# Performance work log

Measured on AMD Instinct MI355X. Metric: run time of the kernel, lower is better.

## Reference

```python
import jax, jax.numpy as jnp
import numpy as np

DIM = 768
HEADS = 12
HIDDEN = 4 * DIM
B, N = 8, 1024
EPS = 1e-5


def setup_inputs() -> dict:
    key = jax.random.key(0)
    ks = jax.random.split(key, 8)
    s = 0.02
    return {
        "x": jax.random.normal(ks[0], (B, N, DIM), dtype=jnp.float32),
        "ln1_g": jnp.ones((DIM,), jnp.float32),
        "ln1_b": jnp.zeros((DIM,), jnp.float32),
        "qkv_w": jax.random.normal(ks[1], (3 * DIM, DIM), jnp.float32) * s,
        "proj_w": jax.random.normal(ks[2], (DIM, DIM), jnp.float32) * s,
        "proj_b": jnp.zeros((DIM,), jnp.float32),
        "ln2_g": jnp.ones((DIM,), jnp.float32),
        "ln2_b": jnp.zeros((DIM,), jnp.float32),
        "fc1_w": jax.random.normal(ks[3], (HIDDEN, DIM), jnp.float32) * s,
        "fc1_b": jnp.zeros((HIDDEN,), jnp.float32),
        "fc2_w": jax.random.normal(ks[4], (DIM, HIDDEN), jnp.float32) * s,
        "fc2_b": jnp.zeros((DIM,), jnp.float32),
    }


def _layernorm(x, g, b):
    mu = jnp.mean(x, axis=-1, keepdims=True)
    var = jnp.mean(jnp.square(x - mu), axis=-1, keepdims=True)
    return (x - mu) * jax.lax.rsqrt(var + EPS) * g + b


def reference(x, ln1_g, ln1_b, qkv_w, proj_w, proj_b, ln2_g, ln2_b, fc1_w, fc1_b, fc2_w, fc2_b):
    Bn, Nn, C = x.shape
    H = HEADS
    D = C // H
    scale = D ** -0.5

    # --- attention branch ---
    h = _layernorm(x, ln1_g, ln1_b)
    qkv = h @ qkv_w.T                      # [B,N,3C] (qkv_bias=False)
    qkv = qkv.reshape(Bn, Nn, 3, H, D)
    q = qkv[:, :, 0].transpose(0, 2, 1, 3)  # [B,H,N,D]
    k = qkv[:, :, 1].transpose(0, 2, 1, 3)
    v = qkv[:, :, 2].transpose(0, 2, 1, 3)
    attn = jnp.einsum('bhnd,bhmd->bhnm', q, k) * scale  # [B,H,N,N]
    attn = jax.nn.softmax(attn, axis=-1)
    ctx = jnp.einsum('bhnm,bhmd->bhnd', attn, v)         # [B,H,N,D]
    ctx = ctx.transpose(0, 2, 1, 3).reshape(Bn, Nn, C)
    x = x + ctx @ proj_w.T + proj_b

    # --- MLP branch ---
    h = _layernorm(x, ln2_g, ln2_b)
    h = jax.nn.gelu(h @ fc1_w.T + fc1_b, approximate=False)
    return x + h @ fc2_w.T + fc2_b
```

## Files before the change

### kernel.cpp

```cpp
#include <hip/hip_runtime.h>
#include <cstdint>

typedef __attribute__((ext_vector_type(8))) short short8;
typedef __attribute__((ext_vector_type(4))) float f32x4;
typedef unsigned short u16t;

__device__ __forceinline__ u16t f2bf(float f) {
  uint32_t u = __float_as_uint(f);
  u += 0x7fffu + ((u >> 16) & 1u);
  return (u16t)(u >> 16);
}

__device__ __forceinline__ uint32_t cvtpk(float lo, float hi) {
  uint32_t r;
  asm("v_cvt_pk_bf16_f32 %0, %1, %2" : "=v"(r) : "v"(lo), "v"(hi));
  return r;
}

__device__ __forceinline__ void gload_lds16(const void* g, void* l) {
  __builtin_amdgcn_global_load_lds(
      (const __attribute__((address_space(1))) void*)g,
      (__attribute__((address_space(3))) void*)l, 16, 0, 0);
}

__global__ __launch_bounds__(256) void cvt_bf16_kernel(const float* __restrict__ in,
                                                       u16t* __restrict__ out, int n8) {
  int i = blockIdx.x * 256 + threadIdx.x;
  if (i >= n8) return;
  const float4* p = (const float4*)in + (size_t)i * 2;
  float4 a = p[0], b = p[1];
  union { short8 v; u16t e[8]; } r;
  r.e[0] = f2bf(a.x); r.e[1] = f2bf(a.y); r.e[2] = f2bf(a.z); r.e[3] = f2bf(a.w);
  r.e[4] = f2bf(b.x); r.e[5] = f2bf(b.y); r.e[6] = f2bf(b.z); r.e[7] = f2bf(b.w);
  *((short8*)out + i) = r.v;
}

__global__ __launch_bounds__(256) void ln_kernel(const float* __restrict__ x,
                                                 const float* __restrict__ g,
                                                 const float* __restrict__ b,
                                                 u16t* __restrict__ out) {
  int row = blockIdx.x, tid = threadIdx.x;
  int wave = tid >> 6, lane = tid & 63;
  const float* xr = x + (size_t)row * 768;
  float v0 = xr[tid], v1 = xr[tid + 256], v2 = xr[tid + 512];
  float s = v0 + v1 + v2;
  float q = v0 * v0 + v1 * v1 + v2 * v2;
#pragma unroll
  for (int m = 32; m >= 1; m >>= 1) {
    s += __shfl_xor(s, m, 64);
    q += __shfl_xor(q, m, 64);
  }
  __shared__ float red[8];
  if (lane == 0) { red[wave] = s; red[4 + wave] = q; }
  __syncthreads();
  s = red[0] + red[1] + red[2] + red[3];
  q = red[4] + red[5] + red[6] + red[7];
  float mu = s * (1.0f / 768.0f);
  float var = q * (1.0f / 768.0f) - mu * mu;
  float rs = rsqrtf(var + 1e-5f);
  u16t* orow = out + (size_t)row * 768;
  orow[tid]       = f2bf((v0 - mu) * rs * g[tid]       + b[tid]);
  orow[tid + 256] = f2bf((v1 - mu) * rs * g[tid + 256] + b[tid + 256]);
  orow[tid + 512] = f2bf((v2 - mu) * rs * g[tid + 512] + b[tid + 512]);
}

template <int EPI, int BM>
__global__ __launch_bounds__(256, 2) void gemm_bt(const u16t* __restrict__ A,
                                                  const u16t* __restrict__ W,
                                                  void* __restrict__ Cout,
                                                  const float* __restrict__ bias,
                                                  const float* __restrict__ res,
                                                  int M, int N, int K) {
  __shared__ __align__(16) u16t As[BM * 64];
  __shared__ __align__(16) u16t Bs[128 * 64];
  constexpr int MF = BM / 32;
  int tid = threadIdx.x;
  int wave = tid >> 6, lane = tid & 63;
  int wr = wave >> 1, wc = wave & 1;
  int bm = blockIdx.y * BM;
  int bn = blockIdx.x * 128;
  f32x4 acc[MF][4] = {};

  int lr = lane >> 3;
  int lc = lane & 7;
  int srcslot = lc ^ lr;
  const u16t* Abase = A + (size_t)(bm + lr) * K + srcslot * 8;
  const u16t* Wbase = W + (size_t)(bn + lr) * K + srcslot * 8;

  for (int kt = 0; kt < K; kt += 64) {
    __syncthreads();
#pragma unroll
    for (int i = 0; i < BM / 32; i++) {
      int chunk = wave * (BM / 32) + i;
      gload_lds16(Abase + (size_t)(chunk * 8) * K + kt, (void*)(As + chunk * 512));
    }
#pragma unroll
    for (int i = 0; i < 4; i++) {
      int chunk = wave * 4 + i;
      gload_lds16(Wbase + (size_t)(chunk * 8) * K + kt, (void*)(Bs + chunk * 512));
    }
    __syncthreads();

    short8 af[MF][2], bfr[4][2];
#pragma unroll
    for (int m = 0; m < MF; m++) {
      int row = wr * (BM / 2) + m * 16 + (lane & 15);
#pragma unroll
      for (int s = 0; s < 2; s++) {
        int slot = s * 4 + (lane >> 4);
        af[m][s] = *(const short8*)(As + row * 64 + ((slot ^ (row & 7)) * 8));
      }
    }
#pragma unroll
    for (int n = 0; n < 4; n++) {
      int row = wc * 64 + n * 16 + (lane & 15);
#pragma unroll
      for (int s = 0; s < 2; s++) {
        int slot = s * 4 + (lane >> 4);
        bfr[n][s] = *(const short8*)(Bs + row * 64 + ((slot ^ (row & 7)) * 8));
      }
    }
    __builtin_amdgcn_s_setprio(1);
#pragma unroll
    for (int m = 0; m < MF; m++)
#pragma unroll
      for (int n = 0; n < 4; n++) {
        acc[m][n] = __builtin_amdgcn_mfma_f32_16x16x32_bf16(af[m][0], bfr[n][0], acc[m][n], 0, 0, 0);
        acc[m][n] = __builtin_amdgcn_mfma_f32_16x16x32_bf16(af[m][1], bfr[n][1], acc[m][n], 0, 0, 0);
      }
    __builtin_amdgcn_s_setprio(0);
  }

#pragma unroll
  for (int m = 0; m < MF; m++) {
#pragma unroll
    for (int n = 0; n < 4; n++) {
      int r0 = bm + wr * (BM / 2) + m * 16 + (lane >> 4) * 4;
      int c = bn + wc * 64 + n * 16 + (lane & 15);
#pragma unroll
      for (int i = 0; i < 4; i++) {
        int r = r0 + i;
        float v = acc[m][n][i];
        if constexpr (EPI == 0) {
          ((u16t*)Cout)[(size_t)r * N + c] = f2bf(v);
        } else if constexpr (EPI == 1) {
          ((float*)Cout)[(size_t)r * N + c] = v + bias[c] + res[(size_t)r * N + c];
        } else {
          v += bias[c];
          float gl = 0.5f * v * (1.0f + erff(v * 0.70710678118f));
          ((u16t*)Cout)[(size_t)r * N + c] = f2bf(gl);
        }
      }
    }
  }
}

__global__ __launch_bounds__(256) void vtrans_kernel(const u16t* __restrict__ qkv,
                                                     u16t* __restrict__ vt) {
  __shared__ u16t T[64][66];
  int h = blockIdx.x % 12, bb = blockIdx.x / 12, kt = blockIdx.y * 64;
  int t = threadIdx.x;
  int r = t >> 2, dc = t & 3;
  const u16t* src = qkv + (size_t)(bb * 1024 + kt + r) * 2304 + 1536 + h * 64 + dc * 16;
  union { uint4 u[2]; u16t e[16]; uint32_t w[8]; } buf;
  buf.u[0] = *(const uint4*)src;
  buf.u[1] = *(const uint4*)(src + 8);
#pragma unroll
  for (int j = 0; j < 8; j++)
    *(uint32_t*)&T[r][dc * 16 + 2 * j] = buf.w[j];
  __syncthreads();
  int d = t >> 2, kc = t & 3;
  union { uint4 u[2]; u16t e[16]; } o;
#pragma unroll
  for (int j = 0; j < 16; j++) o.e[j] = T[kc * 16 + j][d];
  u16t* dst = vt + ((size_t)blockIdx.x * 64 + d) * 1024 + kt + kc * 16;
  *(uint4*)dst = o.u[0];
  *(uint4*)(dst + 8) = o.u[1];
}

__global__ __launch_bounds__(256, 3) void attn_kernel(const u16t* __restrict__ qkv,
                                                      const u16t* __restrict__ vt,
                                                      u16t* __restrict__ ctx) {
  __shared__ __align__(16) u16t Plds[4][32 * 72];
  int tid = threadIdx.x;
  int wave = tid >> 6, lane = tid & 63;
  int q = lane & 15, g = lane >> 4;

  int bid = blockIdx.x;
  int xcd = bid & 7, j = bid >> 3;
  int head = xcd + 8 * (j >> 3);
  int qt = (j & 7) * 128 + wave * 32;
  int b = head / 12, h = head % 12;

  const u16t* base = qkv + (size_t)b * 1024 * 2304 + h * 64;
  const u16t* kbase = base + 768;
  const u16t* vtb = vt + (size_t)head * 64 * 1024;

  short8 qf[2][2];
#pragma unroll
  for (int hf = 0; hf < 2; hf++)
#pragma unroll
    for (int hh = 0; hh < 2; hh++)
      qf[hf][hh] = *(const short8*)(base + (size_t)(qt + hf * 16 + q) * 2304 + hh * 32 + g * 8);

  float mA = -1e30f, mB = -1e30f, lA = 0.f, lB = 0.f;
  f32x4 oA[4] = {}, oB[4] = {};
  u16t* Pw = Plds[wave];

  for (int kt = 0; kt < 1024; kt += 64) {
    short8 kf[4][2], vf[4][2];
#pragma unroll
    for (int n = 0; n < 4; n++)
#pragma unroll
      for (int hh = 0; hh < 2; hh++)
        kf[n][hh] = *(const short8*)(kbase + (size_t)(kt + n * 16 + q) * 2304 + hh * 32 + g * 8);
#pragma unroll
    for (int n = 0; n < 4; n++)
#pragma unroll
      for (int hh = 0; hh < 2; hh++)
        vf[n][hh] = *(const short8*)(vtb + (size_t)(n * 16 + q) * 1024 + kt + hh * 32 + g * 8);

    f32x4 sA[4] = {}, sB[4] = {};
    __builtin_amdgcn_s_setprio(1);
#pragma unroll
    for (int n = 0; n < 4; n++) {
      sA[n] = __builtin_amdgcn_mfma_f32_16x16x32_bf16(kf[n][0], qf[0][0], sA[n], 0, 0, 0);
      sA[n] = __builtin_amdgcn_mfma_f32_16x16x32_bf16(kf[n][1], qf[0][1], sA[n], 0, 0, 0);
      sB[n] = __builtin_amdgcn_mfma_f32_16x16x32_bf16(kf[n][0], qf[1][0], sB[n], 0, 0, 0);
      sB[n] = __builtin_amdgcn_mfma_f32_16x16x32_bf16(kf[n][1], qf[1][1], sB[n], 0, 0, 0);
    }
    __builtin_amdgcn_s_setprio(0);

    float alphaA, alphaB;
    {
      float tm = sA[0][0];
#pragma unroll
      for (int n = 0; n < 4; n++)
#pragma unroll
        for (int i = 0; i < 4; i++) tm = fmaxf(tm, sA[n][i]);
      tm = fmaxf(tm, __shfl_xor(tm, 16, 64));
      tm = fmaxf(tm, __shfl_xor(tm, 32, 64));
      float mnew = fmaxf(mA, tm);
      alphaA = __expf((mA - mnew) * 0.125f);
      mA = mnew;
      float rs = 0.f;
#pragma unroll
      for (int n = 0; n < 4; n++)
#pragma unroll
        for (int i = 0; i < 4; i++) {
          float p = __expf((sA[n][i] - mnew) * 0.125f);
          sA[n][i] = p;
          rs += p;
        }
      rs += __shfl_xor(rs, 16, 64);
      rs += __shfl_xor(rs, 32, 64);
      lA = lA * alphaA + rs;
#pragma unroll
      for (int n = 0; n < 4; n++) {
        uint32_t w0 = cvtpk(sA[n][0], sA[n][1]);
        uint32_t w1 = cvtpk(sA[n][2], sA[n][3]);
        *(uint2*)(Pw + q * 72 + n * 16 + g * 4) = make_uint2(w0, w1);
      }
    }
    {
      float tm = sB[0][0];
#pragma unroll
      for (int n = 0; n < 4; n++)
#pragma unroll
        for (int i = 0; i < 4; i++) tm = fmaxf(tm, sB[n][i]);
      tm = fmaxf(tm, __shfl_xor(tm, 16, 64));
      tm = fmaxf(tm, __shfl_xor(tm, 32, 64));
      float mnew = fmaxf(mB, tm);
      alphaB = __expf((mB - mnew) * 0.125f);
      mB = mnew;
      float rs = 0.f;
#pragma unroll
      for (int n = 0; n < 4; n++)
#pragma unroll
        for (int i = 0; i < 4; i++) {
          float p = __expf((sB[n][i] - mnew) * 0.125f);
          sB[n][i] = p;
          rs += p;
        }
      rs += __shfl_xor(rs, 16, 64);
      rs += __shfl_xor(rs, 32, 64);
      lB = lB * alphaB + rs;
#pragma unroll
      for (int n = 0; n < 4; n++) {
        uint32_t w0 = cvtpk(sB[n][0], sB[n][1]);
        uint32_t w1 = cvtpk(sB[n][2], sB[n][3]);
        *(uint2*)(Pw + (16 + q) * 72 + n * 16 + g * 4) = make_uint2(w0, w1);
      }
    }

#pragma unroll
    for (int n = 0; n < 4; n++)
#pragma unroll
      for (int i = 0; i < 4; i++) {
        oA[n][i] *= alphaA;
        oB[n][i] *= alphaB;
      }

    short8 pA[2], pB[2];
#pragma unroll
    for (int hh = 0; hh < 2; hh++) {
      pA[hh] = *(const short8*)(Pw + q * 72 + hh * 32 + g * 8);
      pB[hh] = *(const short8*)(Pw + (16 + q) * 72 + hh * 32 + g * 8);
    }
    __builtin_amdgcn_s_setprio(1);
#pragma unroll
    for (int n = 0; n < 4; n++)
#pragma unroll
      for (int hh = 0; hh < 2; hh++) {
        oA[n] = __builtin_amdgcn_mfma_f32_16x16x32_bf16(vf[n][hh], pA[hh], oA[n], 0, 0, 0);
        oB[n] = __builtin_amdgcn_mfma_f32_16x16x32_bf16(vf[n][hh], pB[hh], oB[n], 0, 0, 0);
      }
    __builtin_amdgcn_s_setprio(0);
  }

  float invA = 1.f / lA, invB = 1.f / lB;
  u16t* crowA = ctx + (size_t)(b * 1024 + qt + q) * 768 + h * 64;
  u16t* crowB = ctx + (size_t)(b * 1024 + qt + 16 + q) * 768 + h * 64;
#pragma unroll
  for (int n = 0; n < 4; n++) {
    uint32_t a0 = (uint32_t)f2bf(oA[n][0] * invA) | ((uint32_t)f2bf(oA[n][1] * invA) << 16);
    uint32_t a1 = (uint32_t)f2bf(oA[n][2] * invA) | ((uint32_t)f2bf(oA[n][3] * invA) << 16);
    *(uint32_t*)(crowA + n * 16 + g * 4) = a0;
    *(uint32_t*)(crowA + n * 16 + g * 4 + 2) = a1;
    uint32_t b0 = (uint32_t)f2bf(oB[n][0] * invB) | ((uint32_t)f2bf(oB[n][1] * invB) << 16);
    uint32_t b1 = (uint32_t)f2bf(oB[n][2] * invB) | ((uint32_t)f2bf(oB[n][3] * invB) << 16);
    *(uint32_t*)(crowB + n * 16 + g * 4) = b0;
    *(uint32_t*)(crowB + n * 16 + g * 4 + 2) = b1;
  }
}

extern "C" void kernel_launch(void* const* d_in, const int* in_sizes, int n_in,
                              void* d_out, int out_size, void* d_ws, size_t ws_size,
                              hipStream_t stream) {
  const float* x      = (const float*)d_in[0];
  const float* ln1_g  = (const float*)d_in[1];
  const float* ln1_b  = (const float*)d_in[2];
  const float* qkv_w  = (const float*)d_in[3];
  const float* proj_w = (const float*)d_in[4];
  const float* proj_b = (const float*)d_in[5];
  const float* ln2_g  = (const float*)d_in[6];
  const float* ln2_b  = (const float*)d_in[7];
  const float* fc1_w  = (const float*)d_in[8];
  const float* fc1_b  = (const float*)d_in[9];
  const float* fc2_w  = (const float*)d_in[10];
  const float* fc2_b  = (const float*)d_in[11];

  char* ws = (char*)d_ws;
  u16t* h1   = (u16t*)(ws + 0);
  u16t* qkvb = (u16t*)(ws + 12582912);
  u16t* ctx  = (u16t*)(ws + 50331648);
  float* x2  = (float*)(ws + 62914560);
  u16t* hid  = (u16t*)(ws + 88080384);
  u16t* wq   = (u16t*)(ws + 138412032);
  u16t* wp   = (u16t*)(ws + 141950976);
  u16t* w1   = (u16t*)(ws + 143130624);
  u16t* w2   = (u16t*)(ws + 147849216);
  u16t* vtb  = h1;
  float* out = (float*)d_out;

  cvt_bf16_kernel<<<864, 256, 0, stream>>>(qkv_w, wq, 221184);
  cvt_bf16_kernel<<<288, 256, 0, stream>>>(proj_w, wp, 73728);
  cvt_bf16_kernel<<<1152, 256, 0, stream>>>(fc1_w, w1, 294912);
  cvt_bf16_kernel<<<1152, 256, 0, stream>>>(fc2_w, w2, 294912);

  ln_kernel<<<8192, 256, 0, stream>>>(x, ln1_g, ln1_b, h1);
  gemm_bt<0, 128><<<dim3(18, 64), 256, 0, stream>>>(h1, wq, qkvb, nullptr, nullptr, 8192, 2304, 768);
  vtrans_kernel<<<dim3(96, 16), 256, 0, stream>>>(qkvb, vtb);
  attn_kernel<<<768, 256, 0, stream>>>(qkvb, vtb, ctx);
  gemm_bt<1, 64><<<dim3(6, 128), 256, 0, stream>>>(ctx, wp, x2, proj_b, x, 8192, 768, 768);
  ln_kernel<<<8192, 256, 0, stream>>>(x2, ln2_g, ln2_b, h1);
  gemm_bt<2, 128><<<dim3(24, 64), 256, 0, stream>>>(h1, w1, hid, fc1_b, nullptr, 8192, 3072, 768);
  gemm_bt<1, 64><<<dim3(6, 128), 256, 0, stream>>>(hid, w2, out, fc2_b, x2, 8192, 768, 3072);
}
```

Baseline: 306.5 us.

## Halve attention rows per wave and raise occupancy bounds for attention and GEMMs

Each attention wave now handles 16 query rows instead of 32, doubling the grid and cutting register and LDS use, which permits 4 blocks per CU. The V fragment loads are moved after the QK MFMAs, and the max and sum reductions become trees. GEMM launch bounds are made template parameters and raised to 3 or 4 blocks per CU. The cost is that K and V are reloaded twice as often per query, and the tighter register caps risk spills in the GEMMs.

After: 410.8 us. +34.0%, slower.

```diff
diff --git a/kernel.cpp b/kernel.cpp
--- a/kernel.cpp
+++ b/kernel.cpp
@@ -64,13 +64,13 @@
   orow[tid + 512] = f2bf((v2 - mu) * rs * g[tid + 512] + b[tid + 512]);
 }
 
-template <int EPI, int BM>
-__global__ __launch_bounds__(256, 2) void gemm_bt(const u16t* __restrict__ A,
-                                                  const u16t* __restrict__ W,
-                                                  void* __restrict__ Cout,
-                                                  const float* __restrict__ bias,
-                                                  const float* __restrict__ res,
-                                                  int M, int N, int K) {
+template <int EPI, int BM, int MINB>
+__global__ __launch_bounds__(256, MINB) void gemm_bt(const u16t* __restrict__ A,
+                                                     const u16t* __restrict__ W,
+                                                     void* __restrict__ Cout,
+                                                     const float* __restrict__ bias,
+                                                     const float* __restrict__ res,
+                                                     int M, int N, int K) {
   __shared__ __align__(16) u16t As[BM * 64];
   __shared__ __align__(16) u16t Bs[128 * 64];
   constexpr int MF = BM / 32;
@@ -178,159 +178,114 @@
   *(uint4*)(dst + 8) = o.u[1];
 }
 
-__global__ __launch_bounds__(256, 3) void attn_kernel(const u16t* __restrict__ qkv,
+__global__ __launch_bounds__(256, 4) void attn_kernel(const u16t* __restrict__ qkv,
                                                       const u16t* __restrict__ vt,
                                                       u16t* __restrict__ ctx) {
-  __shared__ __align__(16) u16t Plds[4][32 * 72];
+  __shared__ __align__(16) u16t Plds[4][16 * 72];
   int tid = threadIdx.x;
   int wave = tid >> 6, lane = tid & 63;
   int q = lane & 15, g = lane >> 4;
 
   int bid = blockIdx.x;
   int xcd = bid & 7, j = bid >> 3;
-  int head = xcd + 8 * (j >> 3);
-  int qt = (j & 7) * 128 + wave * 32;
+  int head = xcd + 8 * (j >> 4);
+  int qt = (j & 15) * 64 + wave * 16;
   int b = head / 12, h = head % 12;
 
   const u16t* base = qkv + (size_t)b * 1024 * 2304 + h * 64;
   const u16t* kbase = base + 768;
   const u16t* vtb = vt + (size_t)head * 64 * 1024;
 
-  short8 qf[2][2];
-#pragma unroll
-  for (int hf = 0; hf < 2; hf++)
-#pragma unroll
-    for (int hh = 0; hh < 2; hh++)
-      qf[hf][hh] = *(const short8*)(base + (size_t)(qt + hf * 16 + q) * 2304 + hh * 32 + g * 8);
-
-  float mA = -1e30f, mB = -1e30f, lA = 0.f, lB = 0.f;
-  f32x4 oA[4] = {}, oB[4] = {};
+  short8 qf[2];
+#pragma unroll
+  for (int hh = 0; hh < 2; hh++)
+    qf[hh] = *(const short8*)(base + (size_t)(qt + q) * 2304 + hh * 32 + g * 8);
+
+  float m_ = -1e30f, l_ = 0.f;
+  f32x4 o[4] = {};
   u16t* Pw = Plds[wave];
 
   for (int kt = 0; kt < 1024; kt += 64) {
-    short8 kf[4][2], vf[4][2];
+    short8 kf[4][2];
 #pragma unroll
     for (int n = 0; n < 4; n++)
 #pragma unroll
       for (int hh = 0; hh < 2; hh++)
         kf[n][hh] = *(const short8*)(kbase + (size_t)(kt + n * 16 + q) * 2304 + hh * 32 + g * 8);
+
+    f32x4 s[4] = {};
+    __builtin_amdgcn_s_setprio(1);
+#pragma unroll
+    for (int n = 0; n < 4; n++) {
+      s[n] = __builtin_amdgcn_mfma_f32_16x16x32_bf16(kf[n][0], qf[0], s[n], 0, 0, 0);
+      s[n] = __builtin_amdgcn_mfma_f32_16x16x32_bf16(kf[n][1], qf[1], s[n], 0, 0, 0);
+    }
+    __builtin_amdgcn_s_setprio(0);
+
+    short8 vf[4][2];
 #pragma unroll
     for (int n = 0; n < 4; n++)
 #pragma unroll
       for (int hh = 0; hh < 2; hh++)
         vf[n][hh] = *(const short8*)(vtb + (size_t)(n * 16 + q) * 1024 + kt + hh * 32 + g * 8);
 
-    f32x4 sA[4] = {}, sB[4] = {};
+    float tn0 = fmaxf(fmaxf(s[0][0], s[0][1]), fmaxf(s[0][2], s[0][3]));
+    float tn1 = fmaxf(fmaxf(s[1][0], s[1][1]), fmaxf(s[1][2], s[1][3]));
+    float tn2 = fmaxf(fmaxf(s[2][0], s[2][1]), fmaxf(s[2][2], s[2][3]));
+    float tn3 = fmaxf(fmaxf(s[3][0], s[3][1]), fmaxf(s[3][2], s[3][3]));
+    float tm = fmaxf(fmaxf(tn0, tn1), fmaxf(tn2, tn3));
+    tm = fmaxf(tm, __shfl_xor(tm, 16, 64));
+    tm = fmaxf(tm, __shfl_xor(tm, 32, 64));
+    float mnew = fmaxf(m_, tm);
+    float alpha = __expf((m_ - mnew) * 0.125f);
+    m_ = mnew;
+#pragma unroll
+    for (int n = 0; n < 4; n++)
+#pragma unroll
+      for (int i = 0; i < 4; i++)
+        s[n][i] = __expf((s[n][i] - mnew) * 0.125f);
+    float r0 = (s[0][0] + s[0][1]) + (s[0][2] + s[0][3]);
+    float r1 = (s[1][0] + s[1][1]) + (s[1][2] + s[1][3]);
+    float r2 = (s[2][0] + s[2][1]) + (s[2][2] + s[2][3]);
+    float r3 = (s[3][0] + s[3][1]) + (s[3][2] + s[3][3]);
+    float rs = (r0 + r1) + (r2 + r3);
+    rs += __shfl_xor(rs, 16, 64);
+    rs += __shfl_xor(rs, 32, 64);
+    l_ = l_ * alpha + rs;
+
+#pragma unroll
+    for (int n = 0; n < 4; n++) {
+      uint32_t w0 = cvtpk(s[n][0], s[n][1]);
+      uint32_t w1 = cvtpk(s[n][2], s[n][3]);
+      *(uint2*)(Pw + q * 72 + n * 16 + g * 4) = make_uint2(w0, w1);
+    }
+
+#pragma unroll
+    for (int n = 0; n < 4; n++)
+#pragma unroll
+      for (int i = 0; i < 4; i++) o[n][i] *= alpha;
+
+    short8 pA[2];
+#pragma unroll
+    for (int hh = 0; hh < 2; hh++)
+      pA[hh] = *(const short8*)(Pw + q * 72 + hh * 32 + g * 8);
     __builtin_amdgcn_s_setprio(1);
 #pragma unroll
     for (int n = 0; n < 4; n++) {
-      sA[n] = __builtin_amdgcn_mfma_f32_16x16x32_bf16(kf[n][0], qf[0][0], sA[n], 0, 0, 0);
-      sA[n] = __builtin_amdgcn_mfma_f32_16x16x32_bf16(kf[n][1], qf[0][1], sA[n], 0, 0, 0);
-      sB[n] = __builtin_amdgcn_mfma_f32_16x16x32_bf16(kf[n][0], qf[1][0], sB[n], 0, 0, 0);
-      sB[n] = __builtin_amdgcn_mfma_f32_16x16x32_bf16(kf[n][1], qf[1][1], sB[n], 0, 0, 0);
+      o[n] = __builtin_amdgcn_mfma_f32_16x16x32_bf16(vf[n][0], pA[0], o[n], 0, 0, 0);
+      o[n] = __builtin_amdgcn_mfma_f32_16x16x32_bf16(vf[n][1], pA[1], o[n], 0, 0, 0);
     }
     __builtin_amdgcn_s_setprio(0);
-
-    float alphaA, alphaB;
-    {
-      float tm = sA[0][0];
-#pragma unroll
-      for (int n = 0; n < 4; n++)
-#pragma unroll
-        for (int i = 0; i < 4; i++) tm = fmaxf(tm, sA[n][i]);
-      tm = fmaxf(tm, __shfl_xor(tm, 16, 64));
-      tm = fmaxf(tm, __shfl_xor(tm, 32, 64));
-      float mnew = fmaxf(mA, tm);
-      alphaA = __expf((mA - mnew) * 0.125f);
-      mA = mnew;
-      float rs = 0.f;
-#pragma unroll
-      for (int n = 0; n < 4; n++)
-#pragma unroll
-        for (int i = 0; i < 4; i++) {
-          float p = __expf((sA[n][i] - mnew) * 0.125f);
-          sA[n][i] = p;
-          rs += p;
-        }
-      rs += __shfl_xor(rs, 16, 64);
-      rs += __shfl_xor(rs, 32, 64);
-      lA = lA * alphaA + rs;
-#pragma unroll
-      for (int n = 0; n < 4; n++) {
-        uint32_t w0 = cvtpk(sA[n][0], sA[n][1]);
-        uint32_t w1 = cvtpk(sA[n][2], sA[n][3]);
-        *(uint2*)(Pw + q * 72 + n * 16 + g * 4) = make_uint2(w0, w1);
-      }
-    }
-    {
-      float tm = sB[0][0];
-#pragma unroll
-      for (int n = 0; n < 4; n++)
-#pragma unroll
-        for (int i = 0; i < 4; i++) tm = fmaxf(tm, sB[n][i]);
-      tm = fmaxf(tm, __shfl_xor(tm, 16, 64));
-      tm = fmaxf(tm, __shfl_xor(tm, 32, 64));
-      float mnew = fmaxf(mB, tm);
-      alphaB = __expf((mB - mnew) * 0.125f);
-      mB = mnew;
-      float rs = 0.f;
-#pragma unroll
-      for (int n = 0; n < 4; n++)
-#pragma unroll
-        for (int i = 0; i < 4; i++) {
-          float p = __expf((sB[n][i] - mnew) * 0.125f);
-          sB[n][i] = p;
-          rs += p;
-        }
-      rs += __shfl_xor(rs, 16, 64);
-      rs += __shfl_xor(rs, 32, 64);
-      lB = lB * alphaB + rs;
-#pragma unroll
-      for (int n = 0; n < 4; n++) {
-        uint32_t w0 = cvtpk(sB[n][0], sB[n][1]);
-        uint32_t w1 = cvtpk(sB[n][2], sB[n][3]);
-        *(uint2*)(Pw + (16 + q) * 72 + n * 16 + g * 4) = make_uint2(w0, w1);
-      }
-    }
-
-#pragma unroll
-    for (int n = 0; n < 4; n++)
-#pragma unroll
-      for (int i = 0; i < 4; i++) {
-        oA[n][i] *= alphaA;
-        oB[n][i] *= alphaB;
-      }
-
-    short8 pA[2], pB[2];
-#pragma unroll
-    for (int hh = 0; hh < 2; hh++) {
-      pA[hh] = *(const short8*)(Pw + q * 72 + hh * 32 + g * 8);
-      pB[hh] = *(const short8*)(Pw + (16 + q) * 72 + hh * 32 + g * 8);
-    }
-    __builtin_amdgcn_s_setprio(1);
-#pragma unroll
-    for (int n = 0; n < 4; n++)
-#pragma unroll
-      for (int hh = 0; hh < 2; hh++) {
-        oA[n] = __builtin_amdgcn_mfma_f32_16x16x32_bf16(vf[n][hh], pA[hh], oA[n], 0, 0, 0);
-        oB[n] = __builtin_amdgcn_mfma_f32_16x16x32_bf16(vf[n][hh], pB[hh], oB[n], 0, 0, 0);
-      }
-    __builtin_amdgcn_s_setprio(0);
-  }
-
-  float invA = 1.f / lA, invB = 1.f / lB;
-  u16t* crowA = ctx + (size_t)(b * 1024 + qt + q) * 768 + h * 64;
-  u16t* crowB = ctx + (size_t)(b * 1024 + qt + 16 + q) * 768 + h * 64;
+  }
+
+  float inv = 1.f / l_;
+  u16t* crow = ctx + (size_t)(b * 1024 + qt + q) * 768 + h * 64;
 #pragma unroll
   for (int n = 0; n < 4; n++) {
-    uint32_t a0 = (uint32_t)f2bf(oA[n][0] * invA) | ((uint32_t)f2bf(oA[n][1] * invA) << 16);
-    uint32_t a1 = (uint32_t)f2bf(oA[n][2] * invA) | ((uint32_t)f2bf(oA[n][3] * invA) << 16);
-    *(uint32_t*)(crowA + n * 16 + g * 4) = a0;
-    *(uint32_t*)(crowA + n * 16 + g * 4 + 2) = a1;
-    uint32_t b0 = (uint32_t)f2bf(oB[n][0] * invB) | ((uint32_t)f2bf(oB[n][1] * invB) << 16);
-    uint32_t b1 = (uint32_t)f2bf(oB[n][2] * invB) | ((uint32_t)f2bf(oB[n][3] * invB) << 16);
-    *(uint32_t*)(crowB + n * 16 + g * 4) = b0;
-    *(uint32_t*)(crowB + n * 16 + g * 4 + 2) = b1;
+    uint32_t a0 = (uint32_t)f2bf(o[n][0] * inv) | ((uint32_t)f2bf(o[n][1] * inv) << 16);
+    uint32_t a1 = (uint32_t)f2bf(o[n][2] * inv) | ((uint32_t)f2bf(o[n][3] * inv) << 16);
+    *(uint32_t*)(crow + n * 16 + g * 4) = a0;
+    *(uint32_t*)(crow + n * 16 + g * 4 + 2) = a1;
   }
 }
 
@@ -369,11 +324,11 @@
   cvt_bf16_kernel<<<1152, 256, 0, stream>>>(fc2_w, w2, 294912);
 
   ln_kernel<<<8192, 256, 0, stream>>>(x, ln1_g, ln1_b, h1);
-  gemm_bt<0, 128><<<dim3(18, 64), 256, 0, stream>>>(h1, wq, qkvb, nullptr, nullptr, 8192, 2304, 768);
+  gemm_bt<0, 128, 3><<<dim3(18, 64), 256, 0, stream>>>(h1, wq, qkvb, nullptr, nullptr, 8192, 2304, 768);
   vtrans_kernel<<<dim3(96, 16), 256, 0, stream>>>(qkvb, vtb);
-  attn_kernel<<<768, 256, 0, stream>>>(qkvb, vtb, ctx);
-  gemm_bt<1, 64><<<dim3(6, 128), 256, 0, stream>>>(ctx, wp, x2, proj_b, x, 8192, 768, 768);
+  attn_kernel<<<1536, 256, 0, stream>>>(qkvb, vtb, ctx);
+  gemm_bt<1, 64, 4><<<dim3(6, 128), 256, 0, stream>>>(ctx, wp, x2, proj_b, x, 8192, 768, 768);
   ln_kernel<<<8192, 256, 0, stream>>>(x2, ln2_g, ln2_b, h1);
-  gemm_bt<2, 128><<<dim3(24, 64), 256, 0, stream>>>(h1, w1, hid, fc1_b, nullptr, 8192, 3072, 768);
-  gemm_bt<1, 64><<<dim3(6, 128), 256, 0, stream>>>(hid, w2, out, fc2_b, x2, 8192, 768, 3072);
-}
+  gemm_bt<2, 128, 3><<<dim3(24, 64), 256, 0, stream>>>(h1, w1, hid, fc1_b, nullptr, 8192, 3072, 768);
+  gemm_bt<1, 64, 4><<<dim3(6, 128), 256, 0, stream>>>(hid, w2, out, fc2_b, x2, 8192, 768, 3072);
+}
```

## Stage attention K/V tiles through double-buffered LDS and raise GEMM occupancy bounds

Applied to the files above, without the earlier changes.

The attention kernel now cooperatively copies each 64-key K and V^T tile into double-buffered, XOR-swizzled LDS with global_load_lds while computing on the previous tile. Previously each wave loaded its own K/V fragments from global memory. This removes the fourfold redundant global traffic across the block's waves and overlaps loads with compute, at the cost of 32KB more LDS per block and a barrier per iteration. Softmax max and sum reductions become tree-shaped to shorten dependency chains. GEMM launch_bounds min-blocks are raised to 3 or 4, which may force register spills.

Measured after the change: 265.2 us. -13.5%, faster.

```diff
diff --git a/kernel.cpp b/kernel.cpp
--- a/kernel.cpp
+++ b/kernel.cpp
@@ -64,13 +64,13 @@
   orow[tid + 512] = f2bf((v2 - mu) * rs * g[tid + 512] + b[tid + 512]);
 }
 
-template <int EPI, int BM>
-__global__ __launch_bounds__(256, 2) void gemm_bt(const u16t* __restrict__ A,
-                                                  const u16t* __restrict__ W,
-                                                  void* __restrict__ Cout,
-                                                  const float* __restrict__ bias,
-                                                  const float* __restrict__ res,
-                                                  int M, int N, int K) {
+template <int EPI, int BM, int MINB>
+__global__ __launch_bounds__(256, MINB) void gemm_bt(const u16t* __restrict__ A,
+                                                     const u16t* __restrict__ W,
+                                                     void* __restrict__ Cout,
+                                                     const float* __restrict__ bias,
+                                                     const float* __restrict__ res,
+                                                     int M, int N, int K) {
   __shared__ __align__(16) u16t As[BM * 64];
   __shared__ __align__(16) u16t Bs[128 * 64];
   constexpr int MF = BM / 32;
@@ -181,6 +181,8 @@
 __global__ __launch_bounds__(256, 3) void attn_kernel(const u16t* __restrict__ qkv,
                                                       const u16t* __restrict__ vt,
                                                       u16t* __restrict__ ctx) {
+  __shared__ __align__(16) u16t Ks[2][64 * 64];
+  __shared__ __align__(16) u16t Vs[2][64 * 64];
   __shared__ __align__(16) u16t Plds[4][32 * 72];
   int tid = threadIdx.x;
   int wave = tid >> 6, lane = tid & 63;
@@ -203,55 +205,67 @@
     for (int hh = 0; hh < 2; hh++)
       qf[hf][hh] = *(const short8*)(base + (size_t)(qt + hf * 16 + q) * 2304 + hh * 32 + g * 8);
 
+  int lr = lane >> 3, lc = lane & 7;
+  const u16t* ksrc = kbase + (size_t)lr * 2304 + (size_t)((lc ^ lr) * 8);
+  const u16t* vsrc = vtb + (size_t)lr * 1024 + (size_t)((lc ^ lr) * 8);
+  int c0 = wave * 2, c1 = wave * 2 + 1;
+
+  auto stage = [&](int kt, int buf) {
+    gload_lds16(ksrc + (size_t)(kt + c0 * 8) * 2304, (void*)(Ks[buf] + c0 * 512));
+    gload_lds16(ksrc + (size_t)(kt + c1 * 8) * 2304, (void*)(Ks[buf] + c1 * 512));
+    gload_lds16(vsrc + (size_t)(c0 * 8) * 1024 + kt, (void*)(Vs[buf] + c0 * 512));
+    gload_lds16(vsrc + (size_t)(c1 * 8) * 1024 + kt, (void*)(Vs[buf] + c1 * 512));
+  };
+
   float mA = -1e30f, mB = -1e30f, lA = 0.f, lB = 0.f;
   f32x4 oA[4] = {}, oB[4] = {};
   u16t* Pw = Plds[wave];
 
-  for (int kt = 0; kt < 1024; kt += 64) {
-    short8 kf[4][2], vf[4][2];
-#pragma unroll
-    for (int n = 0; n < 4; n++)
-#pragma unroll
-      for (int hh = 0; hh < 2; hh++)
-        kf[n][hh] = *(const short8*)(kbase + (size_t)(kt + n * 16 + q) * 2304 + hh * 32 + g * 8);
-#pragma unroll
-    for (int n = 0; n < 4; n++)
-#pragma unroll
-      for (int hh = 0; hh < 2; hh++)
-        vf[n][hh] = *(const short8*)(vtb + (size_t)(n * 16 + q) * 1024 + kt + hh * 32 + g * 8);
+  stage(0, 0);
+  __syncthreads();
+
+  for (int t = 0; t < 16; ++t) {
+    int buf = t & 1;
+    if (t < 15) stage((t + 1) * 64, buf ^ 1);
+
+    const u16t* Kb = Ks[buf];
+    const u16t* Vb = Vs[buf];
 
     f32x4 sA[4] = {}, sB[4] = {};
     __builtin_amdgcn_s_setprio(1);
 #pragma unroll
     for (int n = 0; n < 4; n++) {
-      sA[n] = __builtin_amdgcn_mfma_f32_16x16x32_bf16(kf[n][0], qf[0][0], sA[n], 0, 0, 0);
-      sA[n] = __builtin_amdgcn_mfma_f32_16x16x32_bf16(kf[n][1], qf[0][1], sA[n], 0, 0, 0);
-      sB[n] = __builtin_amdgcn_mfma_f32_16x16x32_bf16(kf[n][0], qf[1][0], sB[n], 0, 0, 0);
-      sB[n] = __builtin_amdgcn_mfma_f32_16x16x32_bf16(kf[n][1], qf[1][1], sB[n], 0, 0, 0);
+      int row = n * 16 + q;
+      short8 k0 = *(const short8*)(Kb + row * 64 + ((g ^ (q & 7)) * 8));
+      short8 k1 = *(const short8*)(Kb + row * 64 + (((4 + g) ^ (q & 7)) * 8));
+      sA[n] = __builtin_amdgcn_mfma_f32_16x16x32_bf16(k0, qf[0][0], sA[n], 0, 0, 0);
+      sA[n] = __builtin_amdgcn_mfma_f32_16x16x32_bf16(k1, qf[0][1], sA[n], 0, 0, 0);
+      sB[n] = __builtin_amdgcn_mfma_f32_16x16x32_bf16(k0, qf[1][0], sB[n], 0, 0, 0);
+      sB[n] = __builtin_amdgcn_mfma_f32_16x16x32_bf16(k1, qf[1][1], sB[n], 0, 0, 0);
     }
     __builtin_amdgcn_s_setprio(0);
 
     float alphaA, alphaB;
     {
-      float tm = sA[0][0];
-#pragma unroll
-      for (int n = 0; n < 4; n++)
-#pragma unroll
-        for (int i = 0; i < 4; i++) tm = fmaxf(tm, sA[n][i]);
+      float t0 = fmaxf(fmaxf(sA[0][0], sA[0][1]), fmaxf(sA[0][2], sA[0][3]));
+      float t1 = fmaxf(fmaxf(sA[1][0], sA[1][1]), fmaxf(sA[1][2], sA[1][3]));
+      float t2 = fmaxf(fmaxf(sA[2][0], sA[2][1]), fmaxf(sA[2][2], sA[2][3]));
+      float t3 = fmaxf(fmaxf(sA[3][0], sA[3][1]), fmaxf(sA[3][2], sA[3][3]));
+      float tm = fmaxf(fmaxf(t0, t1), fmaxf(t2, t3));
       tm = fmaxf(tm, __shfl_xor(tm, 16, 64));
       tm = fmaxf(tm, __shfl_xor(tm, 32, 64));
       float mnew = fmaxf(mA, tm);
       alphaA = __expf((mA - mnew) * 0.125f);
       mA = mnew;
-      float rs = 0.f;
 #pragma unroll
       for (int n = 0; n < 4; n++)
 #pragma unroll
-        for (int i = 0; i < 4; i++) {
-          float p = __expf((sA[n][i] - mnew) * 0.125f);
-          sA[n][i] = p;
-          rs += p;
-        }
+        for (int i = 0; i < 4; i++) sA[n][i] = __expf((sA[n][i] - mnew) * 0.125f);
+      float r0 = (sA[0][0] + sA[0][1]) + (sA[0][2] + sA[0][3]);
+      float r1 = (sA[1][0] + sA[1][1]) + (sA[1][2] + sA[1][3]);
+      float r2 = (sA[2][0] + sA[2][1]) + (sA[2][2] + sA[2][3]);
+      float r3 = (sA[3][0] + sA[3][1]) + (sA[3][2] + sA[3][3]);
+      float rs = (r0 + r1) + (r2 + r3);
       rs += __shfl_xor(rs, 16, 64);
       rs += __shfl_xor(rs, 32, 64);
       lA = lA * alphaA + rs;
@@ -263,25 +277,25 @@
       }
     }
     {
-      float tm = sB[0][0];
-#pragma unroll
-      for (int n = 0; n < 4; n++)
-#pragma unroll
-        for (int i = 0; i < 4; i++) tm = fmaxf(tm, sB[n][i]);
+      float t0 = fmaxf(fmaxf(sB[0][0], sB[0][1]), fmaxf(sB[0][2], sB[0][3]));
+      float t1 = fmaxf(fmaxf(sB[1][0], sB[1][1]), fmaxf(sB[1][2], sB[1][3]));
+      float t2 = fmaxf(fmaxf(sB[2][0], sB[2][1]), fmaxf(sB[2][2], sB[2][3]));
+      float t3 = fmaxf(fmaxf(sB[3][0], sB[3][1]), fmaxf(sB[3][2], sB[3][3]));
+      float tm = fmaxf(fmaxf(t0, t1), fmaxf(t2, t3));
       tm = fmaxf(tm, __shfl_xor(tm, 16, 64));
       tm = fmaxf(tm, __shfl_xor(tm, 32, 64));
       float mnew = fmaxf(mB, tm);
       alphaB = __expf((mB - mnew) * 0.125f);
       mB = mnew;
-      float rs = 0.f;
 #pragma unroll
       for (int n = 0; n < 4; n++)
 #pragma unroll
-        for (int i = 0; i < 4; i++) {
-          float p = __expf((sB[n][i] - mnew) * 0.125f);
-          sB[n][i] = p;
-          rs += p;
-        }
+        for (int i = 0; i < 4; i++) sB[n][i] = __expf((sB[n][i] - mnew) * 0.125f);
+      float r0 = (sB[0][0] + sB[0][1]) + (sB[0][2] + sB[0][3]);
+      float r1 = (sB[1][0] + sB[1][1]) + (sB[1][2] + sB[1][3]);
+      float r2 = (sB[2][0] + sB[2][1]) + (sB[2][2] + sB[2][3]);
+      float r3 = (sB[3][0] + sB[3][1]) + (sB[3][2] + sB[3][3]);
+      float rs = (r0 + r1) + (r2 + r3);
       rs += __shfl_xor(rs, 16, 64);
       rs += __shfl_xor(rs, 32, 64);
       lB = lB * alphaB + rs;
@@ -309,13 +323,18 @@
     }
     __builtin_amdgcn_s_setprio(1);
 #pragma unroll
-    for (int n = 0; n < 4; n++)
-#pragma unroll
-      for (int hh = 0; hh < 2; hh++) {
-        oA[n] = __builtin_amdgcn_mfma_f32_16x16x32_bf16(vf[n][hh], pA[hh], oA[n], 0, 0, 0);
-        oB[n] = __builtin_amdgcn_mfma_f32_16x16x32_bf16(vf[n][hh], pB[hh], oB[n], 0, 0, 0);
-      }
+    for (int n = 0; n < 4; n++) {
+      int row = n * 16 + q;
+      short8 v0 = *(const short8*)(Vb + row * 64 + ((g ^ (q & 7)) * 8));
+      short8 v1 = *(const short8*)(Vb + row * 64 + (((4 + g) ^ (q & 7)) * 8));
+      oA[n] = __builtin_amdgcn_mfma_f32_16x16x32_bf16(v0, pA[0], oA[n], 0, 0, 0);
+      oA[n] = __builtin_amdgcn_mfma_f32_16x16x32_bf16(v1, pA[1], oA[n], 0, 0, 0);
+      oB[n] = __builtin_amdgcn_mfma_f32_16x16x32_bf16(v0, pB[0], oB[n], 0, 0, 0);
+      oB[n] = __builtin_amdgcn_mfma_f32_16x16x32_bf16(v1, pB[1], oB[n], 0, 0, 0);
+    }
     __builtin_amdgcn_s_setprio(0);
+
+    __syncthreads();
   }
 
   float invA = 1.f / lA, invB = 1.f / lB;
@@ -369,11 +388,11 @@
   cvt_bf16_kernel<<<1152, 256, 0, stream>>>(fc2_w, w2, 294912);
 
   ln_kernel<<<8192, 256, 0, stream>>>(x, ln1_g, ln1_b, h1);
-  gemm_bt<0, 128><<<dim3(18, 64), 256, 0, stream>>>(h1, wq, qkvb, nullptr, nullptr, 8192, 2304, 768);
+  gemm_bt<0, 128, 3><<<dim3(18, 64), 256, 0, stream>>>(h1, wq, qkvb, nullptr, nullptr, 8192, 2304, 768);
   vtrans_kernel<<<dim3(96, 16), 256, 0, stream>>>(qkvb, vtb);
   attn_kernel<<<768, 256, 0, stream>>>(qkvb, vtb, ctx);
-  gemm_bt<1, 64><<<dim3(6, 128), 256, 0, stream>>>(ctx, wp, x2, proj_b, x, 8192, 768, 768);
+  gemm_bt<1, 64, 4><<<dim3(6, 128), 256, 0, stream>>>(ctx, wp, x2, proj_b, x, 8192, 768, 768);
   ln_kernel<<<8192, 256, 0, stream>>>(x2, ln2_g, ln2_b, h1);
-  gemm_bt<2, 128><<<dim3(24, 64), 256, 0, stream>>>(h1, w1, hid, fc1_b, nullptr, 8192, 3072, 768);
-  gemm_bt<1, 64><<<dim3(6, 128), 256, 0, stream>>>(hid, w2, out, fc2_b, x2, 8192, 768, 3072);
-}
+  gemm_bt<2, 128, 3><<<dim3(24, 64), 256, 0, stream>>>(h1, w1, hid, fc1_b, nullptr, 8192, 3072, 768);
+  gemm_bt<1, 64, 4><<<dim3(6, 128), 256, 0, stream>>>(hid, w2, out, fc2_b, x2, 8192, 768, 3072);
+}
```
